# Kernel tuning notes

Hardware: AMD Instinct MI355X
Metric: run time of the kernel (lower is better)

## Reference

```python
import jax, jax.numpy as jnp
import numpy as np

H = 12  # n_heads

def setup_inputs() -> dict:
    key = jax.random.key(0)
    ks = jax.random.split(key, 7)
    dim = 768
    x = jax.random.normal(ks[0], (2, 8, 4, 256, dim), dtype=jnp.float32)
    s = dim ** -0.5
    Wq = jax.random.normal(ks[1], (dim, dim), dtype=jnp.float32) * s
    bq = jax.random.normal(ks[2], (dim,), dtype=jnp.float32) * 0.01
    Wk = jax.random.normal(ks[3], (dim, dim), dtype=jnp.float32) * s
    bk = jax.random.normal(ks[4], (dim,), dtype=jnp.float32) * 0.01
    Wv = jax.random.normal(ks[5], (dim, dim), dtype=jnp.float32) * s
    bv = jax.random.normal(ks[6], (dim,), dtype=jnp.float32) * 0.01
    return {"x": x, "Wq": Wq, "bq": bq, "Wk": Wk, "bk": bk, "Wv": Wv, "bv": bv}

def _split_heads(y):
    # [b,t,l,p,(h d)] -> [b,t,l,h,p,d]
    b, t, l, p, hd = y.shape
    return y.reshape(b, t, l, p, H, hd // H).transpose(0, 1, 2, 4, 3, 5)

def reference(x, Wq, bq, Wk, bk, Wv, bv):
    dim = x.shape[-1]
    scale = (dim / H) ** -0.5
    q = _split_heads(x @ Wq.T + bq)  # [b,t,l,h,p,d]
    k = _split_heads(x @ Wk.T + bk)
    v = _split_heads(x @ Wv.T + bv)
    dots = jnp.einsum('btlhpd,btlhqd->btlhpq', q, k) * scale
    attn = jax.nn.softmax(dots, axis=-1)
    out = jnp.einsum('btlhpq,btlhqd->btlhpd', attn, v)
    # [b,t,l,h,p,d] -> [b,t,l,p,(h d)]
    b, t, l, h, p, d = out.shape
    return out.transpose(0, 1, 2, 4, 3, 5).reshape(b, t, l, p, h * d)
```

## Files before the change

### kernel.cpp

```cpp
#include <hip/hip_runtime.h>

typedef _Float16 f16;
typedef __attribute__((ext_vector_type(2))) _Float16 f16x2;
typedef __attribute__((ext_vector_type(8))) _Float16 f16x8;
typedef __attribute__((ext_vector_type(4))) float f32x4;

#define MFMA16(a,b,c) __builtin_amdgcn_mfma_f32_16x16x32_f16(a,b,c,0,0,0)

constexpr int NSEQ = 64;
constexpr int P    = 256;
constexpr int DIMF = 768;
constexpr int NH   = 12;
constexpr int DH   = 64;
constexpr int M    = NSEQ * P;
constexpr size_t XSZ = (size_t)M * DIMF;
constexpr size_t WSZ = (size_t)DIMF * DIMF;

__device__ __forceinline__ f16x8 cvt8(const float* p) {
    const float4 u = *(const float4*)p;
    const float4 w = *(const float4*)(p + 4);
    f16x2 a = __builtin_bit_cast(f16x2, __builtin_amdgcn_cvt_pkrtz(u.x, u.y));
    f16x2 b = __builtin_bit_cast(f16x2, __builtin_amdgcn_cvt_pkrtz(u.z, u.w));
    f16x2 c = __builtin_bit_cast(f16x2, __builtin_amdgcn_cvt_pkrtz(w.x, w.y));
    f16x2 d = __builtin_bit_cast(f16x2, __builtin_amdgcn_cvt_pkrtz(w.z, w.w));
    f16x8 r;
    r[0]=a[0]; r[1]=a[1]; r[2]=b[0]; r[3]=b[1];
    r[4]=c[0]; r[5]=c[1]; r[6]=d[0]; r[7]=d[1];
    return r;
}

__device__ __forceinline__ void gload16(const void* g, void* l) {
    __builtin_amdgcn_global_load_lds(
        (const __attribute__((address_space(1))) void*)g,
        (__attribute__((address_space(3))) void*)l, 16, 0, 0);
}

__global__ __launch_bounds__(256) void conv_kernel(
    const float* __restrict__ x,
    const float* __restrict__ Wq, const float* __restrict__ Wk,
    const float* __restrict__ Wv,
    f16* __restrict__ xh, f16* __restrict__ wh)
{
    const size_t i8 = ((size_t)blockIdx.x * 256 + threadIdx.x) * 8;
    if (i8 < XSZ) {
        *(f16x8*)(xh + i8) = cvt8(x + i8);
    } else {
        const size_t j = i8 - XSZ;
        const int mtx = (int)(j / WSZ);
        const size_t r = j - (size_t)mtx * WSZ;
        const float* src = (mtx == 0 ? Wq : mtx == 1 ? Wk : Wv) + r;
        *(f16x8*)(wh + j) = cvt8(src);
    }
}

__global__ __launch_bounds__(512, 1) void proj_gemm(
    const f16* __restrict__ xh, const f16* __restrict__ wh,
    const float* __restrict__ bq, const float* __restrict__ bk,
    const float* __restrict__ bv,
    f16* __restrict__ qout, f16* __restrict__ kout, f16* __restrict__ vt)
{
    __shared__ __align__(16) char smem[131072];
    const int wg = (blockIdx.x & 7) * 72 + (blockIdx.x >> 3);
    const int nt = wg % 9;
    const int mt = wg / 9;
    const int m0 = mt * 256, n0 = nt * 256;

    const int tid  = threadIdx.x;
    const int lane = tid & 63;
    const int wave = tid >> 6;
    const int lr   = lane & 15;
    const int lg   = lane >> 4;
    const int wm   = wave >> 2;
    const int wn   = wave & 3;

    const f16* srcA = xh + (size_t)(m0 + (tid >> 3)) * DIMF + ((tid & 7) ^ ((tid >> 3) & 7)) * 8;
    const f16* srcB = wh + (size_t)(n0 + (tid >> 3)) * DIMF + ((tid & 7) ^ ((tid >> 3) & 7)) * 8;
    char* dA = smem + tid * 16;
    char* dB = smem + 65536 + tid * 16;

    const int swz0 = (lg ^ (lr & 7)) * 16;
    const char* rA = smem + (wm * 64 + lr) * 128;
    const char* rB = smem + 65536 + (wn * 32 + lr) * 128;

    f32x4 acc[2][4][2][2];
    #pragma unroll
    for (int ah = 0; ah < 2; ++ah)
      #pragma unroll
      for (int m = 0; m < 4; ++m)
        #pragma unroll
        for (int bh = 0; bh < 2; ++bh)
          #pragma unroll
          for (int n = 0; n < 2; ++n) acc[ah][m][bh][n] = (f32x4){0.f,0.f,0.f,0.f};

    f16x8 a[4][2], bf0[2][2], bf1[2][2];

    #define ST_A(H, T, B) do {                                                    \
        gload16(srcA + (size_t)((H)*128      ) * DIMF + (T)*64, dA + (B)*32768 + (H)*16384);          \
        gload16(srcA + (size_t)((H)*128 + 64 ) * DIMF + (T)*64, dA + (B)*32768 + (H)*16384 + 8192); } while (0)
    #define ST_B(H, T, B) do {                                                    \
        gload16(srcB + (size_t)((H)*128      ) * DIMF + (T)*64, dB + (B)*32768 + (H)*16384);          \
        gload16(srcB + (size_t)((H)*128 + 64 ) * DIMF + (T)*64, dB + (B)*32768 + (H)*16384 + 8192); } while (0)

    #define RD_A(H, B) do { _Pragma("unroll")                                      \
        for (int m = 0; m < 4; ++m) {                                              \
            a[m][0] = *(const f16x8*)(rA + (B)*32768 + (H)*16384 + m*2048 + swz0);        \
            a[m][1] = *(const f16x8*)(rA + (B)*32768 + (H)*16384 + m*2048 + (swz0^64)); } } while (0)
    #define RD_B(H, B, BF) do { _Pragma("unroll")                                  \
        for (int n = 0; n < 2; ++n) {                                              \
            BF[n][0] = *(const f16x8*)(rB + (B)*32768 + (H)*16384 + n*2048 + swz0);       \
            BF[n][1] = *(const f16x8*)(rB + (B)*32768 + (H)*16384 + n*2048 + (swz0^64)); } } while (0)

    #define CLUSTER(AH, BH, BF) do {                                               \
        __builtin_amdgcn_s_setprio(1);                                             \
        _Pragma("unroll") for (int m = 0; m < 4; ++m)                              \
        _Pragma("unroll") for (int n = 0; n < 2; ++n) {                            \
            acc[AH][m][BH][n] = MFMA16(a[m][0], BF[n][0], acc[AH][m][BH][n]);      \
            acc[AH][m][BH][n] = MFMA16(a[m][1], BF[n][1], acc[AH][m][BH][n]); }    \
        __builtin_amdgcn_s_setprio(0); } while (0)

    #define BAR  __builtin_amdgcn_s_barrier()
    #define LGKM asm volatile("s_waitcnt lgkmcnt(0)" ::: "memory")
    #define SCHB __builtin_amdgcn_sched_barrier(0)
    #define VM(N) asm volatile("s_waitcnt vmcnt(" #N ")" ::: "memory")

    ST_A(0, 0, 0); ST_B(0, 0, 0); ST_B(1, 0, 0); ST_A(1, 0, 0);
    VM(0);
    BAR;

    for (int it = 0; it < 6; ++it) {
        const int T = 2 * it;
        const bool st2 = it < 5;

        RD_A(0, 0); RD_B(0, 0, bf0);
        ST_A(0, T + 1, 1); ST_B(0, T + 1, 1);
        VM(6); BAR; LGKM; SCHB;
        CLUSTER(0, 0, bf0);

        RD_B(1, 0, bf1);
        ST_B(1, T + 1, 1);
        VM(6); BAR; LGKM; SCHB;
        CLUSTER(0, 1, bf1);

        RD_A(1, 0);
        ST_A(1, T + 1, 1);
        BAR; LGKM; SCHB;
        CLUSTER(1, 1, bf1);

        VM(4); BAR; SCHB;
        CLUSTER(1, 0, bf0);

        RD_A(0, 1); RD_B(0, 1, bf0);
        if (st2) { ST_A(0, T + 2, 0); ST_B(0, T + 2, 0); }
        if (st2) { VM(6); } else { VM(2); }
        BAR; LGKM; SCHB;
        CLUSTER(0, 0, bf0);

        RD_B(1, 1, bf1);
        if (st2) ST_B(1, T + 2, 0);
        if (st2) { VM(6); } else { VM(0); }
        BAR; LGKM; SCHB;
        CLUSTER(0, 1, bf1);

        RD_A(1, 1);
        if (st2) ST_A(1, T + 2, 0);
        BAR; LGKM; SCHB;
        CLUSTER(1, 1, bf1);

        VM(4); BAR; SCHB;
        CLUSTER(1, 0, bf0);
    }

    __syncthreads();

    const int mat = nt / 3;
    const int c0  = (nt % 3) * 256;
    const int seq = mt;
    const float* __restrict__ bias = mat == 0 ? bq : mat == 1 ? bk : bv;
    float bb[2][2];
    #pragma unroll
    for (int bh = 0; bh < 2; ++bh)
        #pragma unroll
        for (int n = 0; n < 2; ++n)
            bb[bh][n] = bias[c0 + bh*128 + wn*32 + n*16 + lr];

    f16 (*ep)[264] = (f16 (*)[264])smem;
    #pragma unroll
    for (int hh = 0; hh < 2; ++hh) {
        #pragma unroll
        for (int m = 0; m < 4; ++m)
            #pragma unroll
            for (int bh = 0; bh < 2; ++bh)
                #pragma unroll
                for (int n = 0; n < 2; ++n)
                    #pragma unroll
                    for (int i = 0; i < 4; ++i)
                        ep[wm*64 + m*16 + lg*4 + i][bh*128 + wn*32 + n*16 + lr] =
                            (f16)(acc[hh][m][bh][n][i] + bb[bh][n]);
        __syncthreads();
        if (mat < 2) {
            f16* __restrict__ dst = mat ? kout : qout;
            const int r = tid >> 2;
            #pragma unroll
            for (int s = 0; s < 8; ++s) {
                const int ch = s*4 + (tid & 3);
                const int h  = (nt % 3) * 4 + (ch >> 3);
                const int d0 = (ch & 7) * 8;
                *(f16x8*)(dst + ((size_t)(seq*NH + h)*P + hh*128 + r)*DH + d0) =
                    *(const f16x8*)&ep[r][ch*8];
            }
        } else {
            const int col = tid >> 1, rg = tid & 1;
            const int h = (nt % 3) * 4 + (col >> 6), d = col & 63;
            f16* drow = vt + ((size_t)(seq*NH + h)*DH + d)*P + hh*128 + rg*64;
            #pragma unroll
            for (int u = 0; u < 8; ++u) {
                f16x8 vv;
                #pragma unroll
                for (int uu = 0; uu < 8; ++uu)
                    vv[uu] = ep[rg*64 + u*8 + uu][col];
                *(f16x8*)(drow + u*8) = vv;
            }
        }
        __syncthreads();
    }
    #undef ST_A
    #undef ST_B
    #undef RD_A
    #undef RD_B
    #undef CLUSTER
    #undef BAR
    #undef LGKM
    #undef SCHB
    #undef VM
}

__global__ __launch_bounds__(512) void attn_kernel(
    const f16* __restrict__ q, const f16* __restrict__ k,
    const f16* __restrict__ vt, float* __restrict__ out)
{
    __shared__ __align__(16) char kl[32768];
    __shared__ __align__(16) char vl[32768];
    __shared__ __align__(16) char pl[8][2048];

    const int n = blockIdx.x;
    const int b = (n & 7) * 192 + (n >> 3);
    const int half = b & 1;
    const int head = (b >> 1) % NH;
    const int seq  = b / (2 * NH);

    const int tid  = threadIdx.x;
    const int lane = tid & 63;
    const int wave = tid >> 6;
    const int lr   = lane & 15;
    const int lg   = lane >> 4;

    const f16* qh = q  + (size_t)(seq*NH + head)*P*DH;
    const f16* kh = k  + (size_t)(seq*NH + head)*P*DH;
    const f16* vh = vt + (size_t)(seq*NH + head)*DH*P;

    {
        const int r0 = tid >> 3, ck = tid & 7;
        const int d0 = tid >> 5, cv = tid & 31;
        #pragma unroll
        for (int it = 0; it < 4; ++it) {
            const int row = it * 64 + r0;
            gload16(kh + row * 64 + ((ck ^ (row & 7)) * 8), kl + it * 8192 + tid * 16);
            const int d = it * 16 + d0;
            gload16(vh + d * 256 + (((cv & 24) | ((cv ^ d) & 7)) * 8), vl + it * 8192 + tid * 16);
        }
    }

    const int qr0 = half * 128 + wave * 16;
    const f16x8 aq0 = *(const f16x8*)(qh + (qr0 + lr) * DH + lg * 8);
    const f16x8 aq1 = *(const f16x8*)(qh + (qr0 + lr) * DH + 32 + lg * 8);

    __syncthreads();

    f32x4 s[16];
    #pragma unroll
    for (int t = 0; t < 16; ++t) s[t] = (f32x4){0.f,0.f,0.f,0.f};
    #pragma unroll
    for (int t = 0; t < 16; ++t) {
        const int row = t * 16 + lr;
        const f16x8 b0 = *(const f16x8*)(kl + row * 128 + ((lg ^ (row & 7)) * 16));
        const f16x8 b1 = *(const f16x8*)(kl + row * 128 + (((lg + 4) ^ (row & 7)) * 16));
        s[t] = MFMA16(aq0, b0, s[t]);
        s[t] = MFMA16(aq1, b1, s[t]);
    }

    float mx[4] = {-1e30f, -1e30f, -1e30f, -1e30f};
    #pragma unroll
    for (int t = 0; t < 16; ++t)
        #pragma unroll
        for (int i = 0; i < 4; ++i) mx[i] = fmaxf(mx[i], s[t][i]);
    #pragma unroll
    for (int st = 1; st < 16; st <<= 1)
        #pragma unroll
        for (int i = 0; i < 4; ++i) mx[i] = fmaxf(mx[i], __shfl_xor(mx[i], st));

    const float SCL = 0.125f * 1.44269504088896f;
    float rs[4] = {0.f, 0.f, 0.f, 0.f};
    #pragma unroll
    for (int t = 0; t < 16; ++t)
        #pragma unroll
        for (int i = 0; i < 4; ++i) {
            const float e = exp2f((s[t][i] - mx[i]) * SCL);
            s[t][i] = e;
            rs[i] += e;
        }
    #pragma unroll
    for (int st = 1; st < 16; st <<= 1)
        #pragma unroll
        for (int i = 0; i < 4; ++i) rs[i] += __shfl_xor(rs[i], st);

    char* pw = pl[wave];
    f32x4 o[4];
    #pragma unroll
    for (int t = 0; t < 4; ++t) o[t] = (f32x4){0.f,0.f,0.f,0.f};

    #pragma unroll
    for (int qq = 0; qq < 4; ++qq) {
        #pragma unroll
        for (int tt = 0; tt < 4; ++tt) {
            const int t = qq * 4 + tt;
            #pragma unroll
            for (int i = 0; i < 4; ++i) {
                const int r = lg * 4 + i;
                const int klocal = tt * 16 + lr;
                *(f16*)(pw + r * 128 + ((klocal * 2) ^ ((r & 7) << 4))) = (f16)s[t][i];
            }
        }
        #pragma unroll
        for (int kol = 0; kol < 2; ++kol) {
            const f16x8 ap = *(const f16x8*)(pw + lr * 128 + (((kol * 4 + lg) ^ (lr & 7)) * 16));
            #pragma unroll
            for (int dt = 0; dt < 4; ++dt) {
                const int row = dt * 16 + lr;
                const int ch  = qq * 8 + kol * 4 + lg;
                const f16x8 bv_ = *(const f16x8*)(vl + row * 512 + (((ch & 24) | ((ch ^ row) & 7)) * 16));
                o[dt] = MFMA16(ap, bv_, o[dt]);
            }
        }
    }

    #pragma unroll
    for (int i = 0; i < 4; ++i) rs[i] = 1.f / rs[i];
    float* op = out + ((size_t)seq * P + qr0) * DIMF + head * DH;
    #pragma unroll
    for (int t = 0; t < 4; ++t)
        #pragma unroll
        for (int i = 0; i < 4; ++i)
            op[(lg * 4 + i) * DIMF + t * 16 + lr] = o[t][i] * rs[i];
}

extern "C" void kernel_launch(void* const* d_in, const int* in_sizes, int n_in,
                              void* d_out, int out_size, void* d_ws, size_t ws_size,
                              hipStream_t stream) {
    const float* x  = (const float*)d_in[0];
    const float* Wq = (const float*)d_in[1];
    const float* bq = (const float*)d_in[2];
    const float* Wk = (const float*)d_in[3];
    const float* bk = (const float*)d_in[4];
    const float* Wv = (const float*)d_in[5];
    const float* bv = (const float*)d_in[6];
    float* out = (float*)d_out;

    f16* xh = (f16*)d_out;
    f16* wh = xh + XSZ;

    const size_t QSZ = (size_t)M * DIMF;
    f16* q  = (f16*)d_ws;
    f16* k  = q + QSZ;
    f16* vt = k + QSZ;

    const int convThreads = (int)((XSZ + 3 * WSZ) / 8);
    conv_kernel<<<convThreads / 256, 256, 0, stream>>>(x, Wq, Wk, Wv, xh, wh);
    proj_gemm<<<dim3(576), 512, 0, stream>>>(xh, wh, bq, bk, bv, q, k, vt);
    attn_kernel<<<dim3(NSEQ * NH * 2), 512, 0, stream>>>(q, k, vt, out);
}
```

Before: 120.5 us.

## Restructure projection GEMM into 4-stage K=32 pipeline with persistent 512-block grid

The projection GEMM now streams K in 32-wide slices through a four-deep shared-memory ring, replacing the K=64 double buffer, and splits each step into an A phase and a B phase with loads issued two steps ahead. Each wave now owns a 128x64 output tile, arranged as an 8x4 grid of MFMA tiles instead of the previous split-half layout. The launch drops to 512 blocks that loop over the 576 tiles, so 64 blocks handle a second tile. This aims to deepen latency hiding and cut LDS reads per MFMA, at the cost of a tail where some blocks do twice the work, and more barriers per K.

```diff
diff --git a/kernel.cpp b/kernel.cpp
--- a/kernel.cpp
+++ b/kernel.cpp
@@ -60,11 +60,6 @@
     f16* __restrict__ qout, f16* __restrict__ kout, f16* __restrict__ vt)
 {
     __shared__ __align__(16) char smem[131072];
-    const int wg = (blockIdx.x & 7) * 72 + (blockIdx.x >> 3);
-    const int nt = wg % 9;
-    const int mt = wg / 9;
-    const int m0 = mt * 256, n0 = nt * 256;
-
     const int tid  = threadIdx.x;
     const int lane = tid & 63;
     const int wave = tid >> 6;
@@ -73,165 +68,151 @@
     const int wm   = wave >> 2;
     const int wn   = wave & 3;
 
-    const f16* srcA = xh + (size_t)(m0 + (tid >> 3)) * DIMF + ((tid & 7) ^ ((tid >> 3) & 7)) * 8;
-    const f16* srcB = wh + (size_t)(n0 + (tid >> 3)) * DIMF + ((tid & 7) ^ ((tid >> 3) & 7)) * 8;
-    char* dA = smem + tid * 16;
-    char* dB = smem + 65536 + tid * 16;
-
-    const int swz0 = (lg ^ (lr & 7)) * 16;
-    const char* rA = smem + (wm * 64 + lr) * 128;
-    const char* rB = smem + 65536 + (wn * 32 + lr) * 128;
-
-    f32x4 acc[2][4][2][2];
-    #pragma unroll
-    for (int ah = 0; ah < 2; ++ah)
-      #pragma unroll
-      for (int m = 0; m < 4; ++m)
-        #pragma unroll
-        for (int bh = 0; bh < 2; ++bh)
-          #pragma unroll
-          for (int n = 0; n < 2; ++n) acc[ah][m][bh][n] = (f32x4){0.f,0.f,0.f,0.f};
-
-    f16x8 a[4][2], bf0[2][2], bf1[2][2];
-
-    #define ST_A(H, T, B) do {                                                    \
-        gload16(srcA + (size_t)((H)*128      ) * DIMF + (T)*64, dA + (B)*32768 + (H)*16384);          \
-        gload16(srcA + (size_t)((H)*128 + 64 ) * DIMF + (T)*64, dA + (B)*32768 + (H)*16384 + 8192); } while (0)
-    #define ST_B(H, T, B) do {                                                    \
-        gload16(srcB + (size_t)((H)*128      ) * DIMF + (T)*64, dB + (B)*32768 + (H)*16384);          \
-        gload16(srcB + (size_t)((H)*128 + 64 ) * DIMF + (T)*64, dB + (B)*32768 + (H)*16384 + 8192); } while (0)
-
-    #define RD_A(H, B) do { _Pragma("unroll")                                      \
-        for (int m = 0; m < 4; ++m) {                                              \
-            a[m][0] = *(const f16x8*)(rA + (B)*32768 + (H)*16384 + m*2048 + swz0);        \
-            a[m][1] = *(const f16x8*)(rA + (B)*32768 + (H)*16384 + m*2048 + (swz0^64)); } } while (0)
-    #define RD_B(H, B, BF) do { _Pragma("unroll")                                  \
-        for (int n = 0; n < 2; ++n) {                                              \
-            BF[n][0] = *(const f16x8*)(rB + (B)*32768 + (H)*16384 + n*2048 + swz0);       \
-            BF[n][1] = *(const f16x8*)(rB + (B)*32768 + (H)*16384 + n*2048 + (swz0^64)); } } while (0)
-
-    #define CLUSTER(AH, BH, BF) do {                                               \
-        __builtin_amdgcn_s_setprio(1);                                             \
-        _Pragma("unroll") for (int m = 0; m < 4; ++m)                              \
-        _Pragma("unroll") for (int n = 0; n < 2; ++n) {                            \
-            acc[AH][m][BH][n] = MFMA16(a[m][0], BF[n][0], acc[AH][m][BH][n]);      \
-            acc[AH][m][BH][n] = MFMA16(a[m][1], BF[n][1], acc[AH][m][BH][n]); }    \
-        __builtin_amdgcn_s_setprio(0); } while (0)
+    const int swz   = (lg ^ (lr & 3)) * 16;
+    const int rAoff = (wm * 128 + lr) * 64 + swz;
+    const int rBoff = 65536 + (wn * 64 + lr) * 64 + swz;
+
+    const int wg0 = (blockIdx.x & 7) * 64 + (blockIdx.x >> 3);
 
     #define BAR  __builtin_amdgcn_s_barrier()
     #define LGKM asm volatile("s_waitcnt lgkmcnt(0)" ::: "memory")
     #define SCHB __builtin_amdgcn_sched_barrier(0)
-    #define VM(N) asm volatile("s_waitcnt vmcnt(" #N ")" ::: "memory")
-
-    ST_A(0, 0, 0); ST_B(0, 0, 0); ST_B(1, 0, 0); ST_A(1, 0, 0);
-    VM(0);
-    BAR;
-
-    for (int it = 0; it < 6; ++it) {
-        const int T = 2 * it;
-        const bool st2 = it < 5;
-
-        RD_A(0, 0); RD_B(0, 0, bf0);
-        ST_A(0, T + 1, 1); ST_B(0, T + 1, 1);
-        VM(6); BAR; LGKM; SCHB;
-        CLUSTER(0, 0, bf0);
-
-        RD_B(1, 0, bf1);
-        ST_B(1, T + 1, 1);
-        VM(6); BAR; LGKM; SCHB;
-        CLUSTER(0, 1, bf1);
-
-        RD_A(1, 0);
-        ST_A(1, T + 1, 1);
-        BAR; LGKM; SCHB;
-        CLUSTER(1, 1, bf1);
-
-        VM(4); BAR; SCHB;
-        CLUSTER(1, 0, bf0);
-
-        RD_A(0, 1); RD_B(0, 1, bf0);
-        if (st2) { ST_A(0, T + 2, 0); ST_B(0, T + 2, 0); }
-        if (st2) { VM(6); } else { VM(2); }
-        BAR; LGKM; SCHB;
-        CLUSTER(0, 0, bf0);
-
-        RD_B(1, 1, bf1);
-        if (st2) ST_B(1, T + 2, 0);
-        if (st2) { VM(6); } else { VM(0); }
-        BAR; LGKM; SCHB;
-        CLUSTER(0, 1, bf1);
-
-        RD_A(1, 1);
-        if (st2) ST_A(1, T + 2, 0);
-        BAR; LGKM; SCHB;
-        CLUSTER(1, 1, bf1);
-
-        VM(4); BAR; SCHB;
-        CLUSTER(1, 0, bf0);
-    }
-
-    __syncthreads();
-
-    const int mat = nt / 3;
-    const int c0  = (nt % 3) * 256;
-    const int seq = mt;
-    const float* __restrict__ bias = mat == 0 ? bq : mat == 1 ? bk : bv;
-    float bb[2][2];
-    #pragma unroll
-    for (int bh = 0; bh < 2; ++bh)
-        #pragma unroll
-        for (int n = 0; n < 2; ++n)
-            bb[bh][n] = bias[c0 + bh*128 + wn*32 + n*16 + lr];
-
-    f16 (*ep)[264] = (f16 (*)[264])smem;
-    #pragma unroll
-    for (int hh = 0; hh < 2; ++hh) {
-        #pragma unroll
-        for (int m = 0; m < 4; ++m)
+
+    for (int wg = wg0; wg < 576; wg += 512) {
+        const int nt = wg % 9;
+        const int mt = wg / 9;
+        const int m0 = mt * 256, n0 = nt * 256;
+
+        const f16* srcA = xh + (size_t)(m0 + (tid >> 2)) * DIMF
+                             + (((tid & 3) ^ ((tid >> 2) & 3)) * 8);
+        const f16* srcB = wh + (size_t)(n0 + (tid >> 2)) * DIMF
+                             + (((tid & 3) ^ ((tid >> 2) & 3)) * 8);
+
+        f32x4 acc[8][4];
+        #pragma unroll
+        for (int m = 0; m < 8; ++m)
             #pragma unroll
-            for (int bh = 0; bh < 2; ++bh)
+            for (int n = 0; n < 4; ++n) acc[m][n] = (f32x4){0.f,0.f,0.f,0.f};
+
+        #pragma unroll
+        for (int t0 = 0; t0 < 2; ++t0) {
+            gload16(srcA + t0*32,                      smem + t0*16384 + tid*16);
+            gload16(srcA + t0*32 + (size_t)128*DIMF,   smem + t0*16384 + 8192 + tid*16);
+            gload16(srcB + t0*32,                      smem + 65536 + t0*16384 + tid*16);
+            gload16(srcB + t0*32 + (size_t)128*DIMF,   smem + 65536 + t0*16384 + 8192 + tid*16);
+        }
+        asm volatile("s_waitcnt vmcnt(4)" ::: "memory");
+        BAR;
+
+        f16x8 a[4], bb[4];
+
+        #define PH0(QO, STG, VMW)                                              \
+            _Pragma("unroll")                                                  \
+            for (int m = 0; m < 4; ++m)                                        \
+                a[m] = *(const f16x8*)(smem + (QO) + rAoff + m*1024);          \
+            _Pragma("unroll")                                                  \
+            for (int n = 0; n < 4; ++n)                                        \
+                bb[n] = *(const f16x8*)(smem + (QO) + rBoff + n*1024);         \
+            STG;                                                               \
+            VMW;                                                               \
+            BAR; LGKM; SCHB;                                                   \
+            __builtin_amdgcn_s_setprio(1);                                     \
+            _Pragma("unroll")                                                  \
+            for (int m = 0; m < 4; ++m)                                        \
+                _Pragma("unroll")                                              \
+                for (int n = 0; n < 4; ++n)                                    \
+                    acc[m][n] = MFMA16(a[m], bb[n], acc[m][n]);                \
+            __builtin_amdgcn_s_setprio(0);
+
+        #define PH1(QO, STG)                                                   \
+            _Pragma("unroll")                                                  \
+            for (int m = 0; m < 4; ++m)                                        \
+                a[m] = *(const f16x8*)(smem + (QO) + rAoff + (4+m)*1024);      \
+            STG;                                                               \
+            BAR; LGKM; SCHB;                                                   \
+            __builtin_amdgcn_s_setprio(1);                                     \
+            _Pragma("unroll")                                                  \
+            for (int m = 0; m < 4; ++m)                                        \
+                _Pragma("unroll")                                              \
+                for (int n = 0; n < 4; ++n)                                    \
+                    acc[4+m][n] = MFMA16(a[m], bb[n], acc[4+m][n]);            \
+            __builtin_amdgcn_s_setprio(0);
+
+        for (int T = 0; T < 22; ++T) {
+            const int qo = (T & 3) * 16384;
+            const int so = ((T + 2) & 3) * 16384;
+            const f16* ga = srcA + (size_t)(T + 2) * 32;
+            const f16* gb = srcB + (size_t)(T + 2) * 32;
+            PH0(qo,
+                { gload16(ga, smem + so + tid*16);
+                  gload16(ga + (size_t)128*DIMF, smem + so + 8192 + tid*16); },
+                asm volatile("s_waitcnt vmcnt(6)" ::: "memory"));
+            PH1(qo,
+                { gload16(gb, smem + 65536 + so + tid*16);
+                  gload16(gb + (size_t)128*DIMF, smem + 65536 + so + 8192 + tid*16); });
+        }
+        PH0(2*16384, {}, asm volatile("s_waitcnt vmcnt(4)" ::: "memory"));
+        PH1(2*16384, {});
+        PH0(3*16384, {}, asm volatile("s_waitcnt vmcnt(0)" ::: "memory"));
+        PH1(3*16384, {});
+
+        #undef PH0
+        #undef PH1
+
+        __syncthreads();
+
+        const int mat = nt / 3;
+        const int c0  = (nt % 3) * 256;
+        const int seq = mt;
+        const float* __restrict__ bias = mat == 0 ? bq : mat == 1 ? bk : bv;
+        float bv4[4];
+        #pragma unroll
+        for (int n = 0; n < 4; ++n) bv4[n] = bias[c0 + wn*64 + n*16 + lr];
+
+        f16 (*ep)[264] = (f16 (*)[264])smem;
+        #pragma unroll
+        for (int hh = 0; hh < 2; ++hh) {
+            if (wm == hh) {
                 #pragma unroll
-                for (int n = 0; n < 2; ++n)
+                for (int m = 0; m < 8; ++m)
                     #pragma unroll
-                    for (int i = 0; i < 4; ++i)
-                        ep[wm*64 + m*16 + lg*4 + i][bh*128 + wn*32 + n*16 + lr] =
-                            (f16)(acc[hh][m][bh][n][i] + bb[bh][n]);
-        __syncthreads();
-        if (mat < 2) {
-            f16* __restrict__ dst = mat ? kout : qout;
-            const int r = tid >> 2;
-            #pragma unroll
-            for (int s = 0; s < 8; ++s) {
-                const int ch = s*4 + (tid & 3);
-                const int h  = (nt % 3) * 4 + (ch >> 3);
-                const int d0 = (ch & 7) * 8;
-                *(f16x8*)(dst + ((size_t)(seq*NH + h)*P + hh*128 + r)*DH + d0) =
-                    *(const f16x8*)&ep[r][ch*8];
+                    for (int n = 0; n < 4; ++n)
+                        #pragma unroll
+                        for (int i = 0; i < 4; ++i)
+                            ep[m*16 + lg*4 + i][wn*64 + n*16 + lr] =
+                                (f16)(acc[m][n][i] + bv4[n]);
             }
-        } else {
-            const int col = tid >> 1, rg = tid & 1;
-            const int h = (nt % 3) * 4 + (col >> 6), d = col & 63;
-            f16* drow = vt + ((size_t)(seq*NH + h)*DH + d)*P + hh*128 + rg*64;
-            #pragma unroll
-            for (int u = 0; u < 8; ++u) {
-                f16x8 vv;
+            __syncthreads();
+            if (mat < 2) {
+                f16* __restrict__ dst = mat ? kout : qout;
+                const int r = tid >> 2;
                 #pragma unroll
-                for (int uu = 0; uu < 8; ++uu)
-                    vv[uu] = ep[rg*64 + u*8 + uu][col];
-                *(f16x8*)(drow + u*8) = vv;
+                for (int s = 0; s < 8; ++s) {
+                    const int ch = s*4 + (tid & 3);
+                    const int h  = (nt % 3) * 4 + (ch >> 3);
+                    const int d0 = (ch & 7) * 8;
+                    *(f16x8*)(dst + ((size_t)(seq*NH + h)*P + hh*128 + r)*DH + d0) =
+                        *(const f16x8*)&ep[r][ch*8];
+                }
+            } else {
+                const int col = tid >> 1, rg = tid & 1;
+                const int h = (nt % 3) * 4 + (col >> 6), d = col & 63;
+                f16* drow = vt + ((size_t)(seq*NH + h)*DH + d)*P + hh*128 + rg*64;
+                #pragma unroll
+                for (int u = 0; u < 8; ++u) {
+                    f16x8 vv;
+                    #pragma unroll
+                    for (int uu = 0; uu < 8; ++uu)
+                        vv[uu] = ep[rg*64 + u*8 + uu][col];
+                    *(f16x8*)(drow + u*8) = vv;
+                }
             }
-        }
-        __syncthreads();
-    }
-    #undef ST_A
-    #undef ST_B
-    #undef RD_A
-    #undef RD_B
-    #undef CLUSTER
+            __syncthreads();
+        }
+    }
     #undef BAR
     #undef LGKM
     #undef SCHB
-    #undef VM
 }
 
 __global__ __launch_bounds__(512) void attn_kernel(
@@ -375,6 +356,6 @@
 
     const int convThreads = (int)((XSZ + 3 * WSZ) / 8);
     conv_kernel<<<convThreads / 256, 256, 0, stream>>>(x, Wq, Wk, Wv, xh, wh);
-    proj_gemm<<<dim3(576), 512, 0, stream>>>(xh, wh, bq, bk, bv, q, k, vt);
+    proj_gemm<<<dim3(512), 512, 0, stream>>>(xh, wh, bq, bk, bv, q, k, vt);
     attn_kernel<<<dim3(NSEQ * NH * 2), 512, 0, stream>>>(q, k, vt, out);
 }
```

After: 151.9 us. +26.1%, slower.
